# Kernel optimization log

Measured on AMD Instinct MI355X. Metric: run time of the kernel, lower is better.

Reference implementation:

```python
import jax, jax.numpy as jnp
import numpy as np

N_G = 100000  # gene nodes
N_T = 100000  # trait nodes
E = 500000    # edges per etype
D_IN = 128
D_OUT = 128


def setup_inputs() -> dict:
    key = jax.random.key(0)
    ks = jax.random.split(key, 20)
    inp = {
        "x_gene": jax.random.normal(ks[0], (N_G, D_IN), jnp.float32),
        "x_trait": jax.random.normal(ks[1], (N_T, D_IN), jnp.float32),
        "src_gg": jax.random.randint(ks[2], (E,), 0, N_G, jnp.int32),
        "dst_gg": jax.random.randint(ks[3], (E,), 0, N_G, jnp.int32),
        "src_gt": jax.random.randint(ks[4], (E,), 0, N_G, jnp.int32),
        "dst_gt": jax.random.randint(ks[5], (E,), 0, N_T, jnp.int32),
        "src_tg": jax.random.randint(ks[6], (E,), 0, N_T, jnp.int32),
        "dst_tg": jax.random.randint(ks[7], (E,), 0, N_G, jnp.int32),
    }
    # one SAGEConv per edge type: W_neigh, W_self [D_IN, D_OUT], bias [D_OUT]
    i = 8
    for et in ("gg", "gt", "tg"):
        inp[f"Wn_{et}"] = jax.random.normal(ks[i], (D_IN, D_OUT), jnp.float32) * 0.05; i += 1
        inp[f"Ws_{et}"] = jax.random.normal(ks[i], (D_IN, D_OUT), jnp.float32) * 0.05; i += 1
        inp[f"b_{et}"] = jnp.zeros((D_OUT,), jnp.float32)
    return inp


def _sage(x_src, x_dst, src, dst, Wn, Ws, b, n_dst):
    # DGL SAGEConv with 'mean' aggregator:
    # h_neigh = mean over in-edges of src features (0 if no in-edges)
    msg = x_src[src]                                   # [E, D_IN] gather
    ssum = jax.ops.segment_sum(msg, dst, num_segments=n_dst)      # [n_dst, D_IN]
    deg = jax.ops.segment_sum(jnp.ones((src.shape[0],), x_src.dtype), dst,
                              num_segments=n_dst)
    h_neigh = ssum / jnp.maximum(deg, 1.0)[:, None]
    return x_dst @ Ws + h_neigh @ Wn + b               # [n_dst, D_OUT]


def reference(x_gene, x_trait, src_gg, dst_gg, src_gt, dst_gt, src_tg, dst_tg,
              Wn_gg, Ws_gg, b_gg, Wn_gt, Ws_gt, b_gt, Wn_tg, Ws_tg, b_tg):
    h_gg = _sage(x_gene, x_gene, src_gg, dst_gg, Wn_gg, Ws_gg, b_gg, N_G)
    h_gt = _sage(x_gene, x_trait, src_gt, dst_gt, Wn_gt, Ws_gt, b_gt, N_T)
    h_tg = _sage(x_trait, x_gene, src_tg, dst_tg, Wn_tg, Ws_tg, b_tg, N_G)
    # h_node accumulation: gene is dst of both gg and tg
    h_gene = h_gg + h_tg
    h_trait = h_gt
    return (h_gene, h_trait)
```

## Files before the change

kernel.cpp:

```cpp
#include <hip/hip_runtime.h>
#include <hip/hip_bf16.h>


#define D 128
#define NG 100000
#define NT 100000
#define NSEG (NG + NT + NG)

#define NBUCK 256
#define NPB   ((NSEG + NBUCK - 1) / NBUCK)
#define TILE  4096
#define CAP   8192

typedef __bf16 bf16x8 __attribute__((ext_vector_type(8)));
typedef float f32x16 __attribute__((ext_vector_type(16)));
typedef float v2f __attribute__((ext_vector_type(2)));

static __device__ __forceinline__ unsigned short f2bf(float f) {
    return __builtin_bit_cast(unsigned short, (__bf16)f);
}
static __device__ __forceinline__ float bflo(unsigned int v) {
    return __builtin_bit_cast(float, v << 16);
}
static __device__ __forceinline__ float bfhi(unsigned int v) {
    return __builtin_bit_cast(float, v & 0xffff0000u);
}

__global__ __launch_bounds__(256) void zero_kernel(int* __restrict__ bcursor)
{
    bcursor[threadIdx.x] = 0;
}

static __device__ __forceinline__ int edge_seg(
    int ge, const int* d0, int n0, const int* d1, int n1, const int* d2)
{
    if (ge < n0) return d0[ge];
    if (ge < n0 + n1) return NG + d1[ge - n0];
    return NG + NT + d2[ge - n0 - n1];
}
static __device__ __forceinline__ int edge_src(
    int ge, const int* s0, int n0, const int* s1, int n1, const int* s2)
{
    if (ge < n0) return s0[ge];
    if (ge < n0 + n1) return s1[ge - n0];
    return s2[ge - n0 - n1];
}

#define CVT8 (((NG + 1) + (NT + 1)) * D / 8)
#define SETUP_ITEMS (CVT8 + 6144 + 4096 + 128 + 128)

__global__ __launch_bounds__(256) void setup_scatter_kernel(
    const int* __restrict__ s0, const int* __restrict__ d0, int n0,
    const int* __restrict__ s1, const int* __restrict__ d1, int n1,
    const int* __restrict__ s2, const int* __restrict__ d2, int nE,
    int* __restrict__ bcursor, int2* __restrict__ binned, int nWG,
    const float* __restrict__ xg, const float* __restrict__ xt,
    unsigned short* __restrict__ og, unsigned short* __restrict__ ot,
    const float* __restrict__ Ws_gg, const float* __restrict__ Ws_tg,
    const float* __restrict__ Wn_gg, const float* __restrict__ Wn_tg,
    const float* __restrict__ Ws_gt, const float* __restrict__ Wn_gt,
    const float* __restrict__ b_gg, const float* __restrict__ b_tg,
    const float* __restrict__ b_gt,
    unsigned short* __restrict__ WpG, unsigned short* __restrict__ WpT,
    float* __restrict__ biasG, float* __restrict__ biasT)
{
    __shared__ int2 stage[TILE];
    __shared__ int hist[NBUCK], scn[NBUCK], gbase[NBUCK], lcur[NBUCK];
    const int t = threadIdx.x;

    if ((int)blockIdx.x < nWG) {
        hist[t] = 0;
        __syncthreads();

        const int base = blockIdx.x * TILE;
        int mseg[TILE / 256], msrc[TILE / 256];
#pragma unroll
        for (int j = 0; j < TILE / 256; ++j) {
            const int ge = base + j * 256 + t;
            if (ge < nE) {
                mseg[j] = edge_seg(ge, d0, n0, d1, n1, d2);
                msrc[j] = edge_src(ge, s0, n0, s1, n1, s2);
                atomicAdd(&hist[mseg[j] / NPB], 1);
            } else mseg[j] = -1;
        }
        __syncthreads();

        const int h = hist[t];
        scn[t] = h;
        __syncthreads();
        for (int sh = 1; sh < NBUCK; sh <<= 1) {
            int u = (t >= sh) ? scn[t - sh] : 0;
            __syncthreads();
            scn[t] += u;
            __syncthreads();
        }
        const int excl = scn[t] - h;
        __syncthreads();
        scn[t] = excl;
        lcur[t] = excl;
        if (h) gbase[t] = t * CAP + atomicAdd(&bcursor[t], h);
        __syncthreads();

#pragma unroll
        for (int j = 0; j < TILE / 256; ++j) {
            if (mseg[j] >= 0) {
                const int b = mseg[j] / NPB;
                const int pos = atomicAdd(&lcur[b], 1);
                stage[pos] = make_int2(msrc[j], mseg[j]);
            }
        }
        __syncthreads();

        const int cnt = min(TILE, nE - base);
        for (int slot = t; slot < cnt; slot += 256) {
            const int2 pr = stage[slot];
            const int b = pr.y / NPB;
            const int gpos = gbase[b] + (slot - scn[b]);
            if (gpos < (b + 1) * CAP)
                binned[gpos] = pr;
        }
        return;
    }

    const int gid = (blockIdx.x - nWG) * 256 + t;
    if (gid < CVT8) {
        const int ng8 = (NG + 1) * D / 8;
        const float* x; unsigned short* o; int j, nreal8;
        if (gid < ng8) { x = xg; o = og; j = gid;       nreal8 = NG * D / 8; }
        else           { x = xt; o = ot; j = gid - ng8; nreal8 = NT * D / 8; }
        uint4 v = make_uint4(0, 0, 0, 0);
        if (j < nreal8) {
            const float4 f0 = ((const float4*)x)[j * 2];
            const float4 f1 = ((const float4*)x)[j * 2 + 1];
            v.x = (unsigned int)f2bf(f0.x) | ((unsigned int)f2bf(f0.y) << 16);
            v.y = (unsigned int)f2bf(f0.z) | ((unsigned int)f2bf(f0.w) << 16);
            v.z = (unsigned int)f2bf(f1.x) | ((unsigned int)f2bf(f1.y) << 16);
            v.w = (unsigned int)f2bf(f1.z) | ((unsigned int)f2bf(f1.w) << 16);
        }
        ((uint4*)o)[j] = v;
        return;
    }
    const int g2 = gid - CVT8;
    if (g2 < 6144) {
        const int lane = g2 & 63, nt = (g2 >> 6) & 3, kt = g2 >> 8;
        const int n = nt * 32 + (lane & 31);
        const int kb = kt * 16 + (lane >> 5) * 8;
        unsigned int pk[4];
#pragma unroll
        for (int jj = 0; jj < 4; ++jj) {
            unsigned int w2 = 0;
#pragma unroll
            for (int h = 0; h < 2; ++h) {
                const int k = kb + jj * 2 + h;
                float w;
                if (k < 128)      w = Ws_gg[k * D + n] + Ws_tg[k * D + n];
                else if (k < 256) w = Wn_gg[(k - 128) * D + n];
                else              w = Wn_tg[(k - 256) * D + n];
                w2 |= ((unsigned int)f2bf(w)) << (16 * h);
            }
            pk[jj] = w2;
        }
        *(uint4*)(WpG + (size_t)g2 * 8) = make_uint4(pk[0], pk[1], pk[2], pk[3]);
    } else if (g2 < 6144 + 4096) {
        const int g = g2 - 6144;
        const int lane = g & 63, nt = (g >> 6) & 3, kt = g >> 8;
        const int n = nt * 32 + (lane & 31);
        const int kb = kt * 16 + (lane >> 5) * 8;
        unsigned int pk[4];
#pragma unroll
        for (int jj = 0; jj < 4; ++jj) {
            unsigned int w2 = 0;
#pragma unroll
            for (int h = 0; h < 2; ++h) {
                const int k = kb + jj * 2 + h;
                const float w = (k < 128) ? Ws_gt[k * D + n] : Wn_gt[(k - 128) * D + n];
                w2 |= ((unsigned int)f2bf(w)) << (16 * h);
            }
            pk[jj] = w2;
        }
        *(uint4*)(WpT + (size_t)g * 8) = make_uint4(pk[0], pk[1], pk[2], pk[3]);
    } else if (g2 < 10240 + 128) {
        const int i = g2 - 10240;
        biasG[i] = b_gg[i] + b_tg[i];
    } else if (g2 < 10368 + 128) {
        const int i = g2 - 10368;
        biasT[i] = b_gt[i];
    }
}

__global__ __launch_bounds__(256) void bbuild_kernel(
    const int2* __restrict__ binned, const int* __restrict__ bcursor,
    int* __restrict__ off, int* __restrict__ dend, int* __restrict__ sorted)
{
    constexpr int CH = (NPB + 255) / 256;
    __shared__ int ldeg[NPB];
    __shared__ int loff[NPB];
    __shared__ int psum[256];
    const int t = threadIdx.x;
    const int b = blockIdx.x;
    const int ebase = b * CAP;
    const int ecnt = min(bcursor[b], CAP);

    const int n0 = b * NPB;
    const int NL = min(NSEG - n0, NPB);

    for (int i = t; i < NL; i += 256) ldeg[i] = 0;
    __syncthreads();
    for (int e = t; e < ecnt; e += 256)
        atomicAdd(&ldeg[binned[ebase + e].y - n0], 1);
    __syncthreads();

    int s = 0;
#pragma unroll
    for (int k = 0; k < CH; ++k) {
        const int i = t * CH + k;
        if (i < NL) s += ldeg[i];
    }
    psum[t] = s;
    __syncthreads();
    for (int sh = 1; sh < 256; sh <<= 1) {
        int u = (t >= sh) ? psum[t - sh] : 0;
        __syncthreads();
        psum[t] += u;
        __syncthreads();
    }
    int run = psum[t] - s;
#pragma unroll
    for (int k = 0; k < CH; ++k) {
        const int i = t * CH + k;
        if (i < NL) { loff[i] = run; run += ldeg[i]; }
    }
    __syncthreads();

    for (int i = t; i < NL; i += 256) {
        off[n0 + i]  = ebase + loff[i];
        dend[n0 + i] = ebase + loff[i] + ldeg[i];
    }
    __syncthreads();

    for (int e = t; e < ecnt; e += 256) {
        const int2 pr = binned[ebase + e];
        const int slot = atomicAdd(&loff[pr.y - n0], 1);
        sorted[ebase + slot] = pr.x;
    }
}

__global__ __launch_bounds__(256) void agg_all_kernel(
    const unsigned short* __restrict__ xg, const unsigned short* __restrict__ xt,
    const int* __restrict__ off, const int* __restrict__ dend,
    const int* __restrict__ sorted,
    unsigned short* __restrict__ aggA, unsigned short* __restrict__ aggC,
    unsigned short* __restrict__ aggB)
{
    const int t = threadIdx.x;
    const int node = blockIdx.x * 16 + (t >> 4);
    if (node >= NSEG) return;
    const int l = t & 15;
    const int gb = (t & 63) & ~15;
    const int s0 = off[node];
    const int s1 = dend[node];

    const unsigned short* xb;
    unsigned short* out;
    int local, zrow;
    if (node < NG)           { xb = xg; out = aggA; local = node;           zrow = NG; }
    else if (node < NG + NT) { xb = xg; out = aggC; local = node - NG;      zrow = NG; }
    else                     { xb = xt; out = aggB; local = node - NG - NT; zrow = NT; }

    v2f A0 = (v2f){0.f, 0.f}, A1 = (v2f){0.f, 0.f};
    v2f A2 = (v2f){0.f, 0.f}, A3 = (v2f){0.f, 0.f};

    for (int e = s0; e < s1; e += 16) {
        const int cnt = min(s1 - e, 16);
        const int myidx = sorted[e + min(l, cnt - 1)];
#pragma unroll
        for (int j = 0; j < 16; j += 4) {
            if (j < cnt) {
                const int i0 = __shfl(myidx, gb + j, 64);
                const int i1 = (j + 1 < cnt) ? __shfl(myidx, gb + j + 1, 64) : zrow;
                const int i2 = (j + 2 < cnt) ? __shfl(myidx, gb + j + 2, 64) : zrow;
                const int i3 = (j + 3 < cnt) ? __shfl(myidx, gb + j + 3, 64) : zrow;
                const uint4 v0 = *(const uint4*)(xb + (size_t)i0 * D + l * 8);
                const uint4 v1 = *(const uint4*)(xb + (size_t)i1 * D + l * 8);
                const uint4 v2 = *(const uint4*)(xb + (size_t)i2 * D + l * 8);
                const uint4 v3 = *(const uint4*)(xb + (size_t)i3 * D + l * 8);
                A0 += (v2f){bflo(v0.x), bfhi(v0.x)};
                A1 += (v2f){bflo(v0.y), bfhi(v0.y)};
                A2 += (v2f){bflo(v0.z), bfhi(v0.z)};
                A3 += (v2f){bflo(v0.w), bfhi(v0.w)};
                A0 += (v2f){bflo(v1.x), bfhi(v1.x)};
                A1 += (v2f){bflo(v1.y), bfhi(v1.y)};
                A2 += (v2f){bflo(v1.z), bfhi(v1.z)};
                A3 += (v2f){bflo(v1.w), bfhi(v1.w)};
                A0 += (v2f){bflo(v2.x), bfhi(v2.x)};
                A1 += (v2f){bflo(v2.y), bfhi(v2.y)};
                A2 += (v2f){bflo(v2.z), bfhi(v2.z)};
                A3 += (v2f){bflo(v2.w), bfhi(v2.w)};
                A0 += (v2f){bflo(v3.x), bfhi(v3.x)};
                A1 += (v2f){bflo(v3.y), bfhi(v3.y)};
                A2 += (v2f){bflo(v3.z), bfhi(v3.z)};
                A3 += (v2f){bflo(v3.w), bfhi(v3.w)};
            }
        }
    }

    const float inv = 1.0f / (float)max(s1 - s0, 1);
    uint4 o;
    o.x = (unsigned int)f2bf(A0.x * inv) | ((unsigned int)f2bf(A0.y * inv) << 16);
    o.y = (unsigned int)f2bf(A1.x * inv) | ((unsigned int)f2bf(A1.y * inv) << 16);
    o.z = (unsigned int)f2bf(A2.x * inv) | ((unsigned int)f2bf(A2.y * inv) << 16);
    o.w = (unsigned int)f2bf(A3.x * inv) | ((unsigned int)f2bf(A3.y * inv) << 16);
    *(uint4*)(out + (size_t)local * D + l * 8) = o;
}

__global__ __launch_bounds__(1024) void gemm_all(
    const unsigned short* __restrict__ xbG, const unsigned short* __restrict__ xbT,
    const unsigned short* __restrict__ aggA, const unsigned short* __restrict__ aggB,
    const unsigned short* __restrict__ aggC,
    const unsigned short* __restrict__ WpG, const unsigned short* __restrict__ WpT,
    const float* __restrict__ biasG, const float* __restrict__ biasT,
    float* __restrict__ outG, float* __restrict__ outT, int GB)
{
    __shared__ unsigned short WL[8 * 4 * 64 * 8];
    const int t = threadIdx.x;
    const int wid = t >> 6, lane = t & 63;
    const int lm = lane & 31, l5 = lane >> 5;

    const bool isG = (int)blockIdx.x < GB;
    const int bloc = isG ? blockIdx.x : blockIdx.x - GB;
    const int M = isG ? NG : NT;
    const int nsrc = isG ? 3 : 2;
    const unsigned short* A0 = isG ? xbG : xbT;
    const unsigned short* A1 = isG ? aggA : aggC;
    const unsigned short* A2 = aggB;
    const unsigned short* Wpack = isG ? WpG : WpT;
    const float* bias = isG ? biasG : biasT;
    float* out = isG ? outG : outT;

    const int tile = bloc * 16 + wid;
    const bool active = tile * 32 < M;
    const int m = tile * 32 + lm;

    f32x16 acc[4];
    if (active) {
#pragma unroll
        for (int nt = 0; nt < 4; ++nt) {
#pragma unroll
            for (int q = 0; q < 4; ++q) {
                const float4 bq = *(const float4*)&bias[nt * 32 + 4 * l5 + 8 * q];
                acc[nt][4 * q + 0] = bq.x; acc[nt][4 * q + 1] = bq.y;
                acc[nt][4 * q + 2] = bq.z; acc[nt][4 * q + 3] = bq.w;
            }
        }
    }

    const uint4* wg = (const uint4*)Wpack;
    uint4* wl = (uint4*)WL;

#pragma unroll 1
    for (int s = 0; s < nsrc; ++s) {
        __syncthreads();
        wl[t]        = wg[(size_t)s * 2048 + t];
        wl[t + 1024] = wg[(size_t)s * 2048 + t + 1024];
        __syncthreads();
        if (!active) continue;
        const unsigned short* ag = (s == 0) ? A0 : ((s == 1) ? A1 : A2);
        const unsigned short* ar = ag + (size_t)m * D + l5 * 8;
#pragma unroll
        for (int kt = 0; kt < 8; ++kt) {
            const bf16x8 a = *(const bf16x8*)(ar + kt * 16);
#pragma unroll
            for (int nt = 0; nt < 4; ++nt) {
                const bf16x8 b = *(const bf16x8*)&WL[((kt * 4 + nt) * 64 + lane) * 8];
                acc[nt] = __builtin_amdgcn_mfma_f32_32x32x16_bf16(b, a, acc[nt], 0, 0, 0);
            }
        }
    }

    if (active) {
        float* orow = out + (size_t)m * D;
#pragma unroll
        for (int nt = 0; nt < 4; ++nt) {
            float* p = orow + nt * 32 + 4 * l5;
            *(float4*)(p + 0)  = make_float4(acc[nt][0],  acc[nt][1],  acc[nt][2],  acc[nt][3]);
            *(float4*)(p + 8)  = make_float4(acc[nt][4],  acc[nt][5],  acc[nt][6],  acc[nt][7]);
            *(float4*)(p + 16) = make_float4(acc[nt][8],  acc[nt][9],  acc[nt][10], acc[nt][11]);
            *(float4*)(p + 24) = make_float4(acc[nt][12], acc[nt][13], acc[nt][14], acc[nt][15]);
        }
    }
}

extern "C" void kernel_launch(void* const* d_in, const int* in_sizes, int n_in,
                              void* d_out, int out_size, void* d_ws, size_t ws_size,
                              hipStream_t stream)
{
    const float* x_gene  = (const float*)d_in[0];
    const float* x_trait = (const float*)d_in[1];
    const int* src_gg = (const int*)d_in[2];
    const int* dst_gg = (const int*)d_in[3];
    const int* src_gt = (const int*)d_in[4];
    const int* dst_gt = (const int*)d_in[5];
    const int* src_tg = (const int*)d_in[6];
    const int* dst_tg = (const int*)d_in[7];
    const float* Wn_gg = (const float*)d_in[8];
    const float* Ws_gg = (const float*)d_in[9];
    const float* b_gg  = (const float*)d_in[10];
    const float* Wn_gt = (const float*)d_in[11];
    const float* Ws_gt = (const float*)d_in[12];
    const float* b_gt  = (const float*)d_in[13];
    const float* Wn_tg = (const float*)d_in[14];
    const float* Ws_tg = (const float*)d_in[15];
    const float* b_tg  = (const float*)d_in[16];

    const int nE_gg = in_sizes[2];
    const int nE_gt = in_sizes[4];
    const int nE_tg = in_sizes[6];
    const int nE_total = nE_gg + nE_gt + nE_tg;

    float* out_gene  = (float*)d_out;
    float* out_trait = (float*)d_out + (size_t)NG * D;

    unsigned short* xb_gene  = (unsigned short*)d_ws;
    unsigned short* xb_trait = xb_gene + (size_t)(NG + 1) * D;
    unsigned short* aggA = xb_trait + (size_t)(NT + 1) * D;
    unsigned short* aggB = aggA + (size_t)NG * D;
    unsigned short* aggC = aggB + (size_t)NG * D;
    char* p = (char*)(aggC + (size_t)NT * D);
    unsigned short* WpG = (unsigned short*)p;  p += 24 * 4 * 64 * 8 * sizeof(unsigned short);
    unsigned short* WpT = (unsigned short*)p;  p += 16 * 4 * 64 * 8 * sizeof(unsigned short);
    float* biasG = (float*)p;                  p += D * sizeof(float);
    float* biasT = (float*)p;                  p += D * sizeof(float);
    int* off     = (int*)p;                    p += (size_t)NSEG * sizeof(int);
    int* dend    = (int*)p;                    p += (size_t)NSEG * sizeof(int);
    int* bcursor = (int*)p;                    p += NBUCK * sizeof(int);
    int* sorted  = (int*)p;                    p += (size_t)NBUCK * CAP * sizeof(int);
    int2* binned = (int2*)p;

    zero_kernel<<<1, 256, 0, stream>>>(bcursor);

    const int nWG = (nE_total + TILE - 1) / TILE;
    const int setup_blocks = (SETUP_ITEMS + 255) / 256;
    setup_scatter_kernel<<<nWG + setup_blocks, 256, 0, stream>>>(
        src_gg, dst_gg, nE_gg, src_gt, dst_gt, nE_gt, src_tg, dst_tg,
        nE_total, bcursor, binned, nWG,
        x_gene, x_trait, xb_gene, xb_trait,
        Ws_gg, Ws_tg, Wn_gg, Wn_tg, Ws_gt, Wn_gt, b_gg, b_tg, b_gt,
        WpG, WpT, biasG, biasT);

    bbuild_kernel<<<NBUCK, 256, 0, stream>>>(binned, bcursor, off, dend, sorted);

    agg_all_kernel<<<(NSEG + 15) / 16, 256, 0, stream>>>(
        xb_gene, xb_trait, off, dend, sorted, aggA, aggC, aggB);

    const int GBb = ((NG + 31) / 32 + 15) / 16;
    const int TBb = ((NT + 31) / 32 + 15) / 16;
    gemm_all<<<GBb + TBb, 1024, 0, stream>>>(
        xb_gene, xb_trait, aggA, aggB, aggC, WpG, WpT, biasG, biasT,
        out_gene, out_trait, GBb);
}
```

Before: 176.0 us.

## Replace global bucket atomics with per-workgroup cells and halve GEMM block size

The scatter pass now writes each workgroup's edges for a bucket into a fixed-size private cell and records a per-cell count, instead of reserving space through global atomic cursors. This removes the zero_kernel launch and the global atomics. The bucket build kernel walks the cells serially per thread, which adds uneven per-thread loops and caps each cell at 128 edges, so a skewed edge distribution could drop edges. Separately, the GEMM block shrinks from 1024 to 512 threads with more blocks, and each thread now loads twice as much of the weight tile into shared memory.

```diff
diff --git a/kernel.cpp b/kernel.cpp
--- a/kernel.cpp
+++ b/kernel.cpp
@@ -11,6 +11,7 @@
 #define NPB   ((NSEG + NBUCK - 1) / NBUCK)
 #define TILE  4096
 #define CAP   8192
+#define CAPW  128
 
 typedef __bf16 bf16x8 __attribute__((ext_vector_type(8)));
 typedef float f32x16 __attribute__((ext_vector_type(16)));
@@ -24,11 +25,6 @@
 }
 static __device__ __forceinline__ float bfhi(unsigned int v) {
     return __builtin_bit_cast(float, v & 0xffff0000u);
-}
-
-__global__ __launch_bounds__(256) void zero_kernel(int* __restrict__ bcursor)
-{
-    bcursor[threadIdx.x] = 0;
 }
 
 static __device__ __forceinline__ int edge_seg(
@@ -53,7 +49,7 @@
     const int* __restrict__ s0, const int* __restrict__ d0, int n0,
     const int* __restrict__ s1, const int* __restrict__ d1, int n1,
     const int* __restrict__ s2, const int* __restrict__ d2, int nE,
-    int* __restrict__ bcursor, int2* __restrict__ binned, int nWG,
+    int* __restrict__ cellcnt, int2* __restrict__ binned, int nWG,
     const float* __restrict__ xg, const float* __restrict__ xt,
     unsigned short* __restrict__ og, unsigned short* __restrict__ ot,
     const float* __restrict__ Ws_gg, const float* __restrict__ Ws_tg,
@@ -65,7 +61,7 @@
     float* __restrict__ biasG, float* __restrict__ biasT)
 {
     __shared__ int2 stage[TILE];
-    __shared__ int hist[NBUCK], scn[NBUCK], gbase[NBUCK], lcur[NBUCK];
+    __shared__ int hist[NBUCK], scn[NBUCK], lcur[NBUCK];
     const int t = threadIdx.x;
 
     if ((int)blockIdx.x < nWG) {
@@ -86,6 +82,8 @@
         __syncthreads();
 
         const int h = hist[t];
+        cellcnt[(size_t)t * nWG + blockIdx.x] = min(h, CAPW);
+
         scn[t] = h;
         __syncthreads();
         for (int sh = 1; sh < NBUCK; sh <<= 1) {
@@ -98,7 +96,6 @@
         __syncthreads();
         scn[t] = excl;
         lcur[t] = excl;
-        if (h) gbase[t] = t * CAP + atomicAdd(&bcursor[t], h);
         __syncthreads();
 
 #pragma unroll
@@ -115,9 +112,9 @@
         for (int slot = t; slot < cnt; slot += 256) {
             const int2 pr = stage[slot];
             const int b = pr.y / NPB;
-            const int gpos = gbase[b] + (slot - scn[b]);
-            if (gpos < (b + 1) * CAP)
-                binned[gpos] = pr;
+            const int pic = slot - scn[b];
+            if (pic < CAPW)
+                binned[((size_t)b * nWG + blockIdx.x) * CAPW + pic] = pr;
         }
         return;
     }
@@ -189,7 +186,7 @@
 }
 
 __global__ __launch_bounds__(256) void bbuild_kernel(
-    const int2* __restrict__ binned, const int* __restrict__ bcursor,
+    const int2* __restrict__ binned, const int* __restrict__ cellcnt, int nWG,
     int* __restrict__ off, int* __restrict__ dend, int* __restrict__ sorted)
 {
     constexpr int CH = (NPB + 255) / 256;
@@ -198,16 +195,18 @@
     __shared__ int psum[256];
     const int t = threadIdx.x;
     const int b = blockIdx.x;
-    const int ebase = b * CAP;
-    const int ecnt = min(bcursor[b], CAP);
-
     const int n0 = b * NPB;
     const int NL = min(NSEG - n0, NPB);
 
     for (int i = t; i < NL; i += 256) ldeg[i] = 0;
     __syncthreads();
-    for (int e = t; e < ecnt; e += 256)
-        atomicAdd(&ldeg[binned[ebase + e].y - n0], 1);
+
+    for (int w = t; w < nWG; w += 256) {
+        const int c = min(cellcnt[(size_t)b * nWG + w], CAPW);
+        const int2* cell = binned + ((size_t)b * nWG + w) * CAPW;
+        for (int i = 0; i < c; ++i)
+            atomicAdd(&ldeg[cell[i].y - n0], 1);
+    }
     __syncthreads();
 
     int s = 0;
@@ -232,16 +231,21 @@
     }
     __syncthreads();
 
+    const int ebase = b * CAP;
     for (int i = t; i < NL; i += 256) {
         off[n0 + i]  = ebase + loff[i];
         dend[n0 + i] = ebase + loff[i] + ldeg[i];
     }
     __syncthreads();
 
-    for (int e = t; e < ecnt; e += 256) {
-        const int2 pr = binned[ebase + e];
-        const int slot = atomicAdd(&loff[pr.y - n0], 1);
-        sorted[ebase + slot] = pr.x;
+    for (int w = t; w < nWG; w += 256) {
+        const int c = min(cellcnt[(size_t)b * nWG + w], CAPW);
+        const int2* cell = binned + ((size_t)b * nWG + w) * CAPW;
+        for (int i = 0; i < c; ++i) {
+            const int2 pr = cell[i];
+            const int slot = atomicAdd(&loff[pr.y - n0], 1);
+            sorted[ebase + slot] = pr.x;
+        }
     }
 }
 
@@ -313,7 +317,7 @@
     *(uint4*)(out + (size_t)local * D + l * 8) = o;
 }
 
-__global__ __launch_bounds__(1024) void gemm_all(
+__global__ __launch_bounds__(512) void gemm_all(
     const unsigned short* __restrict__ xbG, const unsigned short* __restrict__ xbT,
     const unsigned short* __restrict__ aggA, const unsigned short* __restrict__ aggB,
     const unsigned short* __restrict__ aggC,
@@ -337,7 +341,7 @@
     const float* bias = isG ? biasG : biasT;
     float* out = isG ? outG : outT;
 
-    const int tile = bloc * 16 + wid;
+    const int tile = bloc * 8 + wid;
     const bool active = tile * 32 < M;
     const int m = tile * 32 + lm;
 
@@ -361,7 +365,9 @@
     for (int s = 0; s < nsrc; ++s) {
         __syncthreads();
         wl[t]        = wg[(size_t)s * 2048 + t];
+        wl[t + 512]  = wg[(size_t)s * 2048 + t + 512];
         wl[t + 1024] = wg[(size_t)s * 2048 + t + 1024];
+        wl[t + 1536] = wg[(size_t)s * 2048 + t + 1536];
         __syncthreads();
         if (!active) continue;
         const unsigned short* ag = (s == 0) ? A0 : ((s == 1) ? A1 : A2);
@@ -416,6 +422,7 @@
     const int nE_gt = in_sizes[4];
     const int nE_tg = in_sizes[6];
     const int nE_total = nE_gg + nE_gt + nE_tg;
+    const int nWG = (nE_total + TILE - 1) / TILE;
 
     float* out_gene  = (float*)d_out;
     float* out_trait = (float*)d_out + (size_t)NG * D;
@@ -432,29 +439,26 @@
     float* biasT = (float*)p;                  p += D * sizeof(float);
     int* off     = (int*)p;                    p += (size_t)NSEG * sizeof(int);
     int* dend    = (int*)p;                    p += (size_t)NSEG * sizeof(int);
-    int* bcursor = (int*)p;                    p += NBUCK * sizeof(int);
     int* sorted  = (int*)p;                    p += (size_t)NBUCK * CAP * sizeof(int);
+    int* cellcnt = (int*)p;                    p += (size_t)NBUCK * nWG * sizeof(int);
     int2* binned = (int2*)p;
 
-    zero_kernel<<<1, 256, 0, stream>>>(bcursor);
-
-    const int nWG = (nE_total + TILE - 1) / TILE;
     const int setup_blocks = (SETUP_ITEMS + 255) / 256;
     setup_scatter_kernel<<<nWG + setup_blocks, 256, 0, stream>>>(
         src_gg, dst_gg, nE_gg, src_gt, dst_gt, nE_gt, src_tg, dst_tg,
-        nE_total, bcursor, binned, nWG,
+        nE_total, cellcnt, binned, nWG,
         x_gene, x_trait, xb_gene, xb_trait,
         Ws_gg, Ws_tg, Wn_gg, Wn_tg, Ws_gt, Wn_gt, b_gg, b_tg, b_gt,
         WpG, WpT, biasG, biasT);
 
-    bbuild_kernel<<<NBUCK, 256, 0, stream>>>(binned, bcursor, off, dend, sorted);
+    bbuild_kernel<<<NBUCK, 256, 0, stream>>>(binned, cellcnt, nWG, off, dend, sorted);
 
     agg_all_kernel<<<(NSEG + 15) / 16, 256, 0, stream>>>(
         xb_gene, xb_trait, off, dend, sorted, aggA, aggC, aggB);
 
-    const int GBb = ((NG + 31) / 32 + 15) / 16;
-    const int TBb = ((NT + 31) / 32 + 15) / 16;
-    gemm_all<<<GBb + TBb, 1024, 0, stream>>>(
+    const int GBb = ((NG + 31) / 32 + 7) / 8;
+    const int TBb = ((NT + 31) / 32 + 7) / 8;
+    gemm_all<<<GBb + TBb, 512, 0, stream>>>(
         xb_gene, xb_trait, aggA, aggB, aggC, WpG, WpT, biasG, biasT,
         out_gene, out_trait, GBb);
 }
```

Measured after the change: 173.9 us, median of 2. No clear change (-1.2%).
